# Kernel optimization log

Hardware: AMD Instinct MI355X
Metric: run time of the kernel (lower is better)

The kernel has to match this reference:

```python
import jax, jax.numpy as jnp
import numpy as np

N_EMBD = 768
N_HEAD = 12
HEAD_DIM = N_EMBD // N_HEAD


def setup_inputs() -> dict:
    key = jax.random.key(0)
    k1, k2, k3, k4, k5 = jax.random.split(key, 5)
    B, T, C = 8, 1024, N_EMBD
    s = 0.02
    return {
        "x": jax.random.normal(k1, (B, T, C), dtype=jnp.float32),
        "w_attn": jax.random.normal(k2, (C, 3 * C), dtype=jnp.float32) * s,
        "b_attn": jnp.zeros((3 * C,), dtype=jnp.float32),
        "w_proj": jax.random.normal(k3, (C, C), dtype=jnp.float32) * s,
        "b_proj": jnp.zeros((C,), dtype=jnp.float32),
    }


def reference(x, w_attn, b_attn, w_proj, b_proj):
    B, T, C = x.shape
    H, D = N_HEAD, HEAD_DIM
    qkv = x @ w_attn + b_attn                      # [B,T,3C]
    q, k, v = jnp.split(qkv, 3, axis=-1)
    # [B,H,T,D]
    q = q.reshape(B, T, H, D).transpose(0, 2, 1, 3)
    k = k.reshape(B, T, H, D).transpose(0, 2, 1, 3)
    v = v.reshape(B, T, H, D).transpose(0, 2, 1, 3)
    att = jnp.einsum("bhqd,bhkd->bhqk", q, k) / jnp.sqrt(jnp.float32(D))
    causal = jnp.tril(jnp.ones((T, T), dtype=bool))
    att = jnp.where(causal[None, None], att, jnp.float32(-jnp.inf))
    att = jax.nn.softmax(att, axis=-1)
    y = jnp.einsum("bhqk,bhkd->bhqd", att, v)      # [B,H,T,D]
    y = y.transpose(0, 2, 1, 3).reshape(B, T, C)
    return y @ w_proj + b_proj
```

## Files before the change

### kernel.cpp

```cpp
#include <hip/hip_runtime.h>
#include <hip/hip_bf16.h>
#include <math.h>
#include <type_traits>

#define BATCH 8
#define SEQ   1024
#define NEMBD 768
#define NHEAD 12
#define HDIM  64
#define TC    (3 * NEMBD)

typedef __attribute__((ext_vector_type(4))) float f32x4;
typedef __attribute__((ext_vector_type(8))) short s16x8;

__device__ __forceinline__ unsigned short f2bf(float f) {
    return __builtin_bit_cast(unsigned short, __float2bfloat16(f));
}

__device__ __forceinline__ void gload_lds16(const void* g, void* l) {
    __builtin_amdgcn_global_load_lds(
        (const __attribute__((address_space(1))) void*)g,
        (__attribute__((address_space(3))) void*)l, 16, 0, 0);
}

__global__ __launch_bounds__(256) void prep_kernel(
    const float* __restrict__ x,
    const float* __restrict__ w_attn,
    const float* __restrict__ w_proj,
    unsigned short* __restrict__ xb,
    unsigned short* __restrict__ waT,
    unsigned short* __restrict__ wpT)
{
    const int bid = blockIdx.x, tid = threadIdx.x;
    if (bid < 3072) {
        const int i = (bid * 256 + tid) * 8;
        float4 a = *(const float4*)(x + i);
        float4 b = *(const float4*)(x + i + 4);
        s16x8 v;
        v[0] = f2bf(a.x); v[1] = f2bf(a.y); v[2] = f2bf(a.z); v[3] = f2bf(a.w);
        v[4] = f2bf(b.x); v[5] = f2bf(b.y); v[6] = f2bf(b.z); v[7] = f2bf(b.w);
        *(s16x8*)(xb + i) = v;
        return;
    }
    __shared__ float t[32][33];
    const float* w; unsigned short* wT; int K, N, bx, by;
    if (bid < 4800) {
        const int r = bid - 3072;
        bx = r % 72; by = r / 72; w = w_attn; wT = waT; K = NEMBD; N = TC;
    } else {
        const int r = bid - 4800;
        bx = r % 24; by = r / 24; w = w_proj; wT = wpT; K = NEMBD; N = NEMBD;
    }
    const int tx = tid & 31, ty = tid >> 5;
    const int n0 = bx * 32, k0 = by * 32;
    #pragma unroll
    for (int i = 0; i < 4; ++i)
        t[ty + i * 8][tx] = w[(size_t)(k0 + ty + i * 8) * N + n0 + tx];
    __syncthreads();
    #pragma unroll
    for (int i = 0; i < 4; ++i)
        wT[(size_t)(n0 + ty + i * 8) * K + k0 + tx] = f2bf(t[tx][ty + i * 8]);
}

__global__ __launch_bounds__(512) void gemm_proj256_kernel(
    const unsigned short* __restrict__ A,
    const unsigned short* __restrict__ Bt,
    const float* __restrict__ bias,
    float* __restrict__ C,
    int M, int N, int K, int nbn)
{
    constexpr int BUF = 24576;
    __shared__ __align__(16) char SM[3 * BUF];

    const int tid  = threadIdx.x;
    const int w    = tid >> 6, lane = tid & 63;
    const int lr   = lane & 15, lg = lane >> 4;
    const int wr   = w >> 1, wc = w & 1;

    const int swz = (blockIdx.x & 7) * (gridDim.x >> 3) + (blockIdx.x >> 3);
    const int bm = (swz / nbn) * 256, bn = (swz % nbn) * 128;

    const int srow = tid >> 2;
    const int gcol = ((tid & 3) ^ ((srow >> 1) & 3)) * 8;
    const unsigned short* Ag = A  + (size_t)(bm + srow) * K + gcol;
    const unsigned short* Bg = Bt + (size_t)(bn + srow) * K + gcol;

    const int NT = K >> 5;

    f32x4 acc[4][4];
    #pragma unroll
    for (int m = 0; m < 4; ++m)
        #pragma unroll
        for (int n = 0; n < 4; ++n) acc[m][n] = (f32x4){0.f, 0.f, 0.f, 0.f};

    auto stage = [&](int t) {
        const int k0 = t << 5;
        char* buf = SM + (t % 3) * BUF;
        gload_lds16(Ag + k0,                   buf + tid * 16);
        gload_lds16(Ag + (size_t)128 * K + k0, buf + 8192 + tid * 16);
        gload_lds16(Bg + k0,                   buf + 16384 + tid * 16);
    };

    stage(0);
    stage(1);
    asm volatile("s_waitcnt vmcnt(3)" ::: "memory");
    __builtin_amdgcn_sched_barrier(0);
    __builtin_amdgcn_s_barrier();
    __builtin_amdgcn_sched_barrier(0);

    for (int t = 0; t < NT; ++t) {
        const char* buf = SM + (t % 3) * BUF;
        const bool more = (t + 2 < NT);
        if (more) stage(t + 2);

        s16x8 af[4], bfr[4];
        #pragma unroll
        for (int m = 0; m < 4; ++m) {
            const int ar = wr * 64 + m * 16 + lr;
            af[m] = *(const s16x8*)(buf + ar * 64 + ((lg ^ ((ar >> 1) & 3)) * 16));
        }
        #pragma unroll
        for (int n = 0; n < 4; ++n) {
            const int br = wc * 64 + n * 16 + lr;
            bfr[n] = *(const s16x8*)(buf + 16384 + br * 64
                                         + ((lg ^ ((br >> 1) & 3)) * 16));
        }

        __builtin_amdgcn_s_setprio(1);
        #pragma unroll
        for (int m = 0; m < 4; ++m)
            #pragma unroll
            for (int n = 0; n < 4; ++n)
                acc[m][n] = __builtin_amdgcn_mfma_f32_16x16x32_bf16(
                    af[m], bfr[n], acc[m][n], 0, 0, 0);
        __builtin_amdgcn_s_setprio(0);

        if (more) asm volatile("s_waitcnt vmcnt(3)" ::: "memory");
        else      asm volatile("s_waitcnt vmcnt(0)" ::: "memory");
        __builtin_amdgcn_sched_barrier(0);
        __builtin_amdgcn_s_barrier();
        __builtin_amdgcn_sched_barrier(0);
    }

    #pragma unroll
    for (int n = 0; n < 4; ++n) {
        const int col = bn + wc * 64 + n * 16 + lr;
        const float bv = bias[col];
        #pragma unroll
        for (int m = 0; m < 4; ++m) {
            const int row0 = bm + wr * 64 + m * 16 + lg * 4;
            #pragma unroll
            for (int r = 0; r < 4; ++r)
                C[(size_t)(row0 + r) * N + col] = acc[m][n][r] + bv;
        }
    }
}

__global__ __launch_bounds__(512) void gemm_qkv256_kernel(
    const unsigned short* __restrict__ A,
    const unsigned short* __restrict__ Bt,
    const float* __restrict__ bias,
    unsigned short* __restrict__ Qb,
    unsigned short* __restrict__ Kb,
    unsigned short* __restrict__ Vtb,
    int M, int K, int nbn)
{
    constexpr int BUF = 24576;
    __shared__ __align__(16) char SM[3 * BUF];

    const int tid  = threadIdx.x;
    const int w    = tid >> 6, lane = tid & 63;
    const int lr   = lane & 15, lg = lane >> 4;
    const int wr   = w >> 1, wc = w & 1;

    const int swz = (blockIdx.x & 7) * (gridDim.x >> 3) + (blockIdx.x >> 3);
    const int bm = (swz / nbn) * 256, bn = (swz % nbn) * 128;

    const int srow = tid >> 2;
    const int gcol = ((tid & 3) ^ ((srow >> 1) & 3)) * 8;
    const unsigned short* Ag = A  + (size_t)(bm + srow) * K + gcol;
    const unsigned short* Bg = Bt + (size_t)(bn + srow) * K + gcol;

    const int NT = K >> 5;

    f32x4 acc[4][4];
    #pragma unroll
    for (int m = 0; m < 4; ++m)
        #pragma unroll
        for (int n = 0; n < 4; ++n) acc[m][n] = (f32x4){0.f, 0.f, 0.f, 0.f};

    auto stage = [&](int t) {
        const int k0 = t << 5;
        char* buf = SM + (t % 3) * BUF;
        gload_lds16(Ag + k0,                   buf + tid * 16);
        gload_lds16(Ag + (size_t)128 * K + k0, buf + 8192 + tid * 16);
        gload_lds16(Bg + k0,                   buf + 16384 + tid * 16);
    };

    stage(0);
    stage(1);
    asm volatile("s_waitcnt vmcnt(3)" ::: "memory");
    __builtin_amdgcn_sched_barrier(0);
    __builtin_amdgcn_s_barrier();
    __builtin_amdgcn_sched_barrier(0);

    for (int t = 0; t < NT; ++t) {
        const char* buf = SM + (t % 3) * BUF;
        const bool more = (t + 2 < NT);
        if (more) stage(t + 2);

        s16x8 af[4], bfr[4];
        #pragma unroll
        for (int m = 0; m < 4; ++m) {
            const int ar = wr * 64 + m * 16 + lr;
            af[m] = *(const s16x8*)(buf + ar * 64 + ((lg ^ ((ar >> 1) & 3)) * 16));
        }
        #pragma unroll
        for (int n = 0; n < 4; ++n) {
            const int br = wc * 64 + n * 16 + lr;
            bfr[n] = *(const s16x8*)(buf + 16384 + br * 64
                                         + ((lg ^ ((br >> 1) & 3)) * 16));
        }

        __builtin_amdgcn_s_setprio(1);
        #pragma unroll
        for (int m = 0; m < 4; ++m)
            #pragma unroll
            for (int n = 0; n < 4; ++n)
                acc[m][n] = __builtin_amdgcn_mfma_f32_16x16x32_bf16(
                    af[m], bfr[n], acc[m][n], 0, 0, 0);
        __builtin_amdgcn_s_setprio(0);

        if (more) asm volatile("s_waitcnt vmcnt(3)" ::: "memory");
        else      asm volatile("s_waitcnt vmcnt(0)" ::: "memory");
        __builtin_amdgcn_sched_barrier(0);
        __builtin_amdgcn_s_barrier();
        __builtin_amdgcn_sched_barrier(0);
    }

    char* Ep = SM + w * 8192;

    const int region = bn / NEMBD;
    const int hh = ((bn % NEMBD) >> 6) + wc;
    const int row0 = bm + wr * 64;
    const int bb = row0 >> 10, t0 = row0 & 1023;
    const float scl = (region == 0) ? 0.1803368801111354f : 1.0f;

    float bvn[4];
    #pragma unroll
    for (int n = 0; n < 4; ++n) bvn[n] = bias[bn + wc * 64 + n * 16 + lr];

    if (region == 2) {
        #pragma unroll
        for (int m = 0; m < 4; ++m)
            #pragma unroll
            for (int n = 0; n < 4; ++n) {
                ushort4 pk;
                pk.x = f2bf(acc[m][n][0] + bvn[n]);
                pk.y = f2bf(acc[m][n][1] + bvn[n]);
                pk.z = f2bf(acc[m][n][2] + bvn[n]);
                pk.w = f2bf(acc[m][n][3] + bvn[n]);
                const int row = n * 16 + lr;
                const int lc  = m * 2 + (lg >> 1);
                *(ushort4*)(Ep + row * 128 + ((lc ^ (lr & 7)) * 16)
                               + (lg & 1) * 8) = pk;
            }
    } else {
        #pragma unroll
        for (int m = 0; m < 4; ++m)
            #pragma unroll
            for (int n = 0; n < 4; ++n)
                #pragma unroll
                for (int r = 0; r < 4; ++r) {
                    const int row = m * 16 + lg * 4 + r;
                    const int lc  = n * 2 + (lr >> 3);
                    *(unsigned short*)(Ep + row * 128
                        + ((lc ^ (row & 7)) * 16) + (lr & 7) * 2) =
                        f2bf((acc[m][n][r] + bvn[n]) * scl);
                }
    }
    asm volatile("s_waitcnt lgkmcnt(0)" ::: "memory");
    __builtin_amdgcn_sched_barrier(0);

    const int rr0 = lane >> 3;
    const int cc  = lane & 7;
    if (region == 2) {
        unsigned short* dst = Vtb + (((size_t)bb * NHEAD + hh) * HDIM) * SEQ + t0;
        #pragma unroll
        for (int it = 0; it < 8; ++it) {
            const int d = it * 8 + rr0;
            s16x8 v = *(const s16x8*)(Ep + d * 128 + ((cc ^ (d & 7)) * 16));
            *(s16x8*)(dst + (size_t)d * SEQ + cc * 8) = v;
        }
    } else {
        unsigned short* dst = (region == 0 ? Qb : Kb)
                            + ((size_t)bb * NHEAD + hh) * SEQ * HDIM;
        #pragma unroll
        for (int it = 0; it < 8; ++it) {
            const int t = it * 8 + rr0;
            s16x8 v = *(const s16x8*)(Ep + t * 128 + ((cc ^ (t & 7)) * 16));
            *(s16x8*)(dst + (size_t)(t0 + t) * HDIM + cc * 8) = v;
        }
    }
}

__global__ __launch_bounds__(256) void attn_mfma_kernel(
    const unsigned short* __restrict__ Qb,
    const unsigned short* __restrict__ Kb,
    const unsigned short* __restrict__ Vtb,
    unsigned short* __restrict__ y)
{
    const int bid  = blockIdx.x;
    const int xcd  = bid & 7;
    const int grp  = bid >> 3;
    const int pair = grp & 7;
    const int bh   = xcd + 8 * (grp >> 3);
    const int b    = bh / NHEAD, h = bh % NHEAD;

    const int tid  = threadIdx.x;
    const int w    = tid >> 6;
    const int lane = tid & 63;
    const int lr   = lane & 15;
    const int lg   = lane >> 4;

    __shared__ __align__(16) unsigned short Ks[2][64 * 72];
    __shared__ __align__(16) unsigned short Vs[2][64 * 72];
    __shared__ __align__(16) unsigned short Ps[4][16][72];

    const unsigned short* Kg = Kb  + (size_t)bh * SEQ * HDIM;
    const unsigned short* Vg = Vtb + (size_t)bh * HDIM * SEQ;

    const int sr = tid >> 2;
    const int sc = (tid & 3) * 16;
    const unsigned short* Kgr = Kg + (size_t)sr * HDIM + sc;
    const unsigned short* Vgr = Vg + (size_t)sr * SEQ  + sc;
    const int woff = sr * 72 + sc;

    auto process = [&](int qt) {
        const unsigned short* Qg =
            Qb + ((size_t)bh * SEQ + qt * 64 + w * 16) * HDIM;
        s16x8 qf[2];
        #pragma unroll
        for (int kc = 0; kc < 2; ++kc)
            qf[kc] = *(const s16x8*)(Qg + (size_t)lr * HDIM + kc * 32 + lg * 8);

        f32x4 acc[4];
        #pragma unroll
        for (int df = 0; df < 4; ++df) acc[df] = (f32x4){0.f, 0.f, 0.f, 0.f};
        float lrow = 0.f;

        const int NT   = qt + 1;
        const int qrow = qt * 64 + w * 16 + lr;

        s16x8 krA = *(const s16x8*)(Kgr);
        s16x8 krB = *(const s16x8*)(Kgr + 8);
        s16x8 vrA = *(const s16x8*)(Vgr);
        s16x8 vrB = *(const s16x8*)(Vgr + 8);

        for (int kt = 0; kt < NT; ++kt) {
            const int cb = kt & 1;
            *(s16x8*)(&Ks[cb][woff])     = krA;
            *(s16x8*)(&Ks[cb][woff] + 8) = krB;
            *(s16x8*)(&Vs[cb][woff])     = vrA;
            *(s16x8*)(&Vs[cb][woff] + 8) = vrB;
            if (kt + 1 < NT) {
                krA = *(const s16x8*)(Kgr + (size_t)(kt + 1) * 64 * HDIM);
                krB = *(const s16x8*)(Kgr + (size_t)(kt + 1) * 64 * HDIM + 8);
                vrA = *(const s16x8*)(Vgr + (kt + 1) * 64);
                vrB = *(const s16x8*)(Vgr + (kt + 1) * 64 + 8);
            }
            asm volatile("s_waitcnt lgkmcnt(0)" ::: "memory");
            __builtin_amdgcn_sched_barrier(0);
            __builtin_amdgcn_s_barrier();
            __builtin_amdgcn_sched_barrier(0);

            f32x4 sf[4];
            __builtin_amdgcn_s_setprio(1);
            #pragma unroll
            for (int s = 0; s < 4; ++s) {
                const unsigned short* kr = &Ks[cb][(s * 16 + lr) * 72 + lg * 8];
                s16x8 a0 = *(const s16x8*)(kr);
                s16x8 a1 = *(const s16x8*)(kr + 32);
                sf[s] = __builtin_amdgcn_mfma_f32_16x16x32_bf16(
                    a0, qf[0], (f32x4){0.f, 0.f, 0.f, 0.f}, 0, 0, 0);
                sf[s] = __builtin_amdgcn_mfma_f32_16x16x32_bf16(a1, qf[1], sf[s], 0, 0, 0);
            }
            __builtin_amdgcn_s_setprio(0);

            float sv[4][4];
            #pragma unroll
            for (int s = 0; s < 4; ++s)
                #pragma unroll
                for (int r = 0; r < 4; ++r)
                    sv[s][r] = sf[s][r];
            if (kt == NT - 1) {
                const int kbase = kt * 64;
                #pragma unroll
                for (int s = 0; s < 4; ++s)
                    #pragma unroll
                    for (int r = 0; r < 4; ++r)
                        if (kbase + s * 16 + lg * 4 + r > qrow)
                            sv[s][r] = -INFINITY;
            }

            #pragma unroll
            for (int s = 0; s < 4; ++s) {
                float p0 = exp2f(sv[s][0]);
                float p1 = exp2f(sv[s][1]);
                float p2 = exp2f(sv[s][2]);
                float p3 = exp2f(sv[s][3]);
                lrow += (p0 + p1) + (p2 + p3);
                ushort4 pk;
                pk.x = f2bf(p0); pk.y = f2bf(p1); pk.z = f2bf(p2); pk.w = f2bf(p3);
                *(ushort4*)&Ps[w][lr][s * 16 + lg * 4] = pk;
            }

            asm volatile("s_waitcnt lgkmcnt(0)" ::: "memory");
            __builtin_amdgcn_sched_barrier(0);
            s16x8 pa[2];
            #pragma unroll
            for (int kc = 0; kc < 2; ++kc)
                pa[kc] = *(const s16x8*)&Ps[w][lr][kc * 32 + lg * 8];

            __builtin_amdgcn_s_setprio(1);
            #pragma unroll
            for (int df = 0; df < 4; ++df) {
                const unsigned short* vr = &Vs[cb][(df * 16 + lr) * 72 + lg * 8];
                s16x8 va0 = *(const s16x8*)(vr);
                s16x8 va1 = *(const s16x8*)(vr + 32);
                acc[df] = __builtin_amdgcn_mfma_f32_16x16x32_bf16(va0, pa[0], acc[df], 0, 0, 0);
                acc[df] = __builtin_amdgcn_mfma_f32_16x16x32_bf16(va1, pa[1], acc[df], 0, 0, 0);
            }
            __builtin_amdgcn_s_setprio(0);
        }

        lrow += __shfl_xor(lrow, 16, 64);
        lrow += __shfl_xor(lrow, 32, 64);
        const float inv = 1.f / lrow;
        const int t = qt * 64 + w * 16 + lr;
        unsigned short* yp = y + ((size_t)(b * SEQ) + t) * NEMBD + h * HDIM;
        #pragma unroll
        for (int df = 0; df < 4; ++df) {
            ushort4 pk;
            pk.x = f2bf(acc[df][0] * inv);
            pk.y = f2bf(acc[df][1] * inv);
            pk.z = f2bf(acc[df][2] * inv);
            pk.w = f2bf(acc[df][3] * inv);
            *(ushort4*)(yp + df * 16 + lg * 4) = pk;
        }
        __builtin_amdgcn_s_barrier();
        __builtin_amdgcn_sched_barrier(0);
    };

    process(15 - pair);
    process(pair);
}

extern "C" void kernel_launch(void* const* d_in, const int* in_sizes, int n_in,
                              void* d_out, int out_size, void* d_ws, size_t ws_size,
                              hipStream_t stream)
{
    const float* x      = (const float*)d_in[0];
    const float* w_attn = (const float*)d_in[1];
    const float* b_attn = (const float*)d_in[2];
    const float* w_proj = (const float*)d_in[3];
    const float* b_proj = (const float*)d_in[4];
    float* out = (float*)d_out;

    const int M = BATCH * SEQ;
    const size_t NQKV = (size_t)M * NEMBD;

    unsigned short* xb  = (unsigned short*)d_ws;
    unsigned short* waT = xb  + NQKV;
    unsigned short* wpT = waT + (size_t)TC * NEMBD;
    unsigned short* Qb  = wpT + (size_t)NEMBD * NEMBD;
    unsigned short* Kb  = Qb  + NQKV;
    unsigned short* Vtb = Kb  + NQKV;
    unsigned short* yb  = Vtb + NQKV;

    prep_kernel<<<5376, 256, 0, stream>>>(x, w_attn, w_proj, xb, waT, wpT);

    gemm_qkv256_kernel<<<(M / 256) * (TC / 128), 512, 0, stream>>>(
        xb, waT, b_attn, Qb, Kb, Vtb, M, NEMBD, TC / 128);

    attn_mfma_kernel<<<768, 256, 0, stream>>>(Qb, Kb, Vtb, yb);

    gemm_proj256_kernel<<<(M / 256) * (NEMBD / 128), 512, 0, stream>>>(
        yb, wpT, b_proj, out, M, NEMBD, NEMBD, NEMBD / 128);
}
```

Baseline: 102.1 us.

## Halve QKV GEMM block to 256 threads with 128x64 per-wave tiles

The QKV GEMM now uses 4 waves of 256 threads, each computing a 128x64 output tile (8x4 MFMA accumulators) instead of 8 waves with 64x64 tiles. Loads are restructured so each thread issues 6 LDS-direct loads per stage, and the wait counts change to match. The epilogue writes the two 64-row halves one after another through the per-wave LDS scratch. The goal is more MFMA work per LDS fragment read and less barrier overhead, at the cost of doubled accumulator registers and a launch bound that targets 2 blocks per CU.

```diff
diff --git a/kernel.cpp b/kernel.cpp
--- a/kernel.cpp
+++ b/kernel.cpp
@@ -156,7 +156,7 @@
     }
 }
 
-__global__ __launch_bounds__(512) void gemm_qkv256_kernel(
+__global__ __launch_bounds__(256, 2) void gemm_qkv256_kernel(
     const unsigned short* __restrict__ A,
     const unsigned short* __restrict__ Bt,
     const float* __restrict__ bias,
@@ -183,23 +183,27 @@
 
     const int NT = K >> 5;
 
-    f32x4 acc[4][4];
-    #pragma unroll
-    for (int m = 0; m < 4; ++m)
+    f32x4 acc[8][4];
+    #pragma unroll
+    for (int m = 0; m < 8; ++m)
         #pragma unroll
         for (int n = 0; n < 4; ++n) acc[m][n] = (f32x4){0.f, 0.f, 0.f, 0.f};
 
     auto stage = [&](int t) {
         const int k0 = t << 5;
         char* buf = SM + (t % 3) * BUF;
-        gload_lds16(Ag + k0,                   buf + tid * 16);
-        gload_lds16(Ag + (size_t)128 * K + k0, buf + 8192 + tid * 16);
-        gload_lds16(Bg + k0,                   buf + 16384 + tid * 16);
+        #pragma unroll
+        for (int p = 0; p < 4; ++p)
+            gload_lds16(Ag + (size_t)(p * 64) * K + k0, buf + p * 4096 + tid * 16);
+        #pragma unroll
+        for (int p = 0; p < 2; ++p)
+            gload_lds16(Bg + (size_t)(p * 64) * K + k0,
+                        buf + 16384 + p * 4096 + tid * 16);
     };
 
     stage(0);
     stage(1);
-    asm volatile("s_waitcnt vmcnt(3)" ::: "memory");
+    asm volatile("s_waitcnt vmcnt(6)" ::: "memory");
     __builtin_amdgcn_sched_barrier(0);
     __builtin_amdgcn_s_barrier();
     __builtin_amdgcn_sched_barrier(0);
@@ -209,10 +213,10 @@
         const bool more = (t + 2 < NT);
         if (more) stage(t + 2);
 
-        s16x8 af[4], bfr[4];
-        #pragma unroll
-        for (int m = 0; m < 4; ++m) {
-            const int ar = wr * 64 + m * 16 + lr;
+        s16x8 af[8], bfr[4];
+        #pragma unroll
+        for (int m = 0; m < 8; ++m) {
+            const int ar = wr * 128 + m * 16 + lr;
             af[m] = *(const s16x8*)(buf + ar * 64 + ((lg ^ ((ar >> 1) & 3)) * 16));
         }
         #pragma unroll
@@ -224,14 +228,14 @@
 
         __builtin_amdgcn_s_setprio(1);
         #pragma unroll
-        for (int m = 0; m < 4; ++m)
+        for (int m = 0; m < 8; ++m)
             #pragma unroll
             for (int n = 0; n < 4; ++n)
                 acc[m][n] = __builtin_amdgcn_mfma_f32_16x16x32_bf16(
                     af[m], bfr[n], acc[m][n], 0, 0, 0);
         __builtin_amdgcn_s_setprio(0);
 
-        if (more) asm volatile("s_waitcnt vmcnt(3)" ::: "memory");
+        if (more) asm volatile("s_waitcnt vmcnt(6)" ::: "memory");
         else      asm volatile("s_waitcnt vmcnt(0)" ::: "memory");
         __builtin_amdgcn_sched_barrier(0);
         __builtin_amdgcn_s_barrier();
@@ -242,64 +246,73 @@
 
     const int region = bn / NEMBD;
     const int hh = ((bn % NEMBD) >> 6) + wc;
-    const int row0 = bm + wr * 64;
-    const int bb = row0 >> 10, t0 = row0 & 1023;
     const float scl = (region == 0) ? 0.1803368801111354f : 1.0f;
 
     float bvn[4];
     #pragma unroll
     for (int n = 0; n < 4; ++n) bvn[n] = bias[bn + wc * 64 + n * 16 + lr];
 
-    if (region == 2) {
-        #pragma unroll
-        for (int m = 0; m < 4; ++m)
-            #pragma unroll
-            for (int n = 0; n < 4; ++n) {
-                ushort4 pk;
-                pk.x = f2bf(acc[m][n][0] + bvn[n]);
-                pk.y = f2bf(acc[m][n][1] + bvn[n]);
-                pk.z = f2bf(acc[m][n][2] + bvn[n]);
-                pk.w = f2bf(acc[m][n][3] + bvn[n]);
-                const int row = n * 16 + lr;
-                const int lc  = m * 2 + (lg >> 1);
-                *(ushort4*)(Ep + row * 128 + ((lc ^ (lr & 7)) * 16)
-                               + (lg & 1) * 8) = pk;
-            }
-    } else {
-        #pragma unroll
-        for (int m = 0; m < 4; ++m)
-            #pragma unroll
-            for (int n = 0; n < 4; ++n)
+    #pragma unroll
+    for (int c = 0; c < 2; ++c) {
+        if (c) {
+            asm volatile("s_waitcnt lgkmcnt(0)" ::: "memory");
+            __builtin_amdgcn_sched_barrier(0);
+        }
+        const int row0 = bm + wr * 128 + c * 64;
+        const int bb = row0 >> 10, t0 = row0 & 1023;
+
+        if (region == 2) {
+            #pragma unroll
+            for (int m4 = 0; m4 < 4; ++m4)
                 #pragma unroll
-                for (int r = 0; r < 4; ++r) {
-                    const int row = m * 16 + lg * 4 + r;
-                    const int lc  = n * 2 + (lr >> 3);
-                    *(unsigned short*)(Ep + row * 128
-                        + ((lc ^ (row & 7)) * 16) + (lr & 7) * 2) =
-                        f2bf((acc[m][n][r] + bvn[n]) * scl);
+                for (int n = 0; n < 4; ++n) {
+                    const f32x4 a = acc[c * 4 + m4][n];
+                    ushort4 pk;
+                    pk.x = f2bf(a[0] + bvn[n]);
+                    pk.y = f2bf(a[1] + bvn[n]);
+                    pk.z = f2bf(a[2] + bvn[n]);
+                    pk.w = f2bf(a[3] + bvn[n]);
+                    const int row = n * 16 + lr;
+                    const int lc  = m4 * 2 + (lg >> 1);
+                    *(ushort4*)(Ep + row * 128 + ((lc ^ (lr & 7)) * 16)
+                                   + (lg & 1) * 8) = pk;
                 }
-    }
-    asm volatile("s_waitcnt lgkmcnt(0)" ::: "memory");
-    __builtin_amdgcn_sched_barrier(0);
-
-    const int rr0 = lane >> 3;
-    const int cc  = lane & 7;
-    if (region == 2) {
-        unsigned short* dst = Vtb + (((size_t)bb * NHEAD + hh) * HDIM) * SEQ + t0;
-        #pragma unroll
-        for (int it = 0; it < 8; ++it) {
-            const int d = it * 8 + rr0;
-            s16x8 v = *(const s16x8*)(Ep + d * 128 + ((cc ^ (d & 7)) * 16));
-            *(s16x8*)(dst + (size_t)d * SEQ + cc * 8) = v;
-        }
-    } else {
-        unsigned short* dst = (region == 0 ? Qb : Kb)
-                            + ((size_t)bb * NHEAD + hh) * SEQ * HDIM;
-        #pragma unroll
-        for (int it = 0; it < 8; ++it) {
-            const int t = it * 8 + rr0;
-            s16x8 v = *(const s16x8*)(Ep + t * 128 + ((cc ^ (t & 7)) * 16));
-            *(s16x8*)(dst + (size_t)(t0 + t) * HDIM + cc * 8) = v;
+        } else {
+            #pragma unroll
+            for (int m4 = 0; m4 < 4; ++m4)
+                #pragma unroll
+                for (int n = 0; n < 4; ++n)
+                    #pragma unroll
+                    for (int r = 0; r < 4; ++r) {
+                        const int row = m4 * 16 + lg * 4 + r;
+                        const int lc  = n * 2 + (lr >> 3);
+                        *(unsigned short*)(Ep + row * 128
+                            + ((lc ^ (row & 7)) * 16) + (lr & 7) * 2) =
+                            f2bf((acc[c * 4 + m4][n][r] + bvn[n]) * scl);
+                    }
+        }
+        asm volatile("s_waitcnt lgkmcnt(0)" ::: "memory");
+        __builtin_amdgcn_sched_barrier(0);
+
+        const int rr0 = lane >> 3;
+        const int cc  = lane & 7;
+        if (region == 2) {
+            unsigned short* dst = Vtb + (((size_t)bb * NHEAD + hh) * HDIM) * SEQ + t0;
+            #pragma unroll
+            for (int it = 0; it < 8; ++it) {
+                const int d = it * 8 + rr0;
+                s16x8 v = *(const s16x8*)(Ep + d * 128 + ((cc ^ (d & 7)) * 16));
+                *(s16x8*)(dst + (size_t)d * SEQ + cc * 8) = v;
+            }
+        } else {
+            unsigned short* dst = (region == 0 ? Qb : Kb)
+                                + ((size_t)bb * NHEAD + hh) * SEQ * HDIM;
+            #pragma unroll
+            for (int it = 0; it < 8; ++it) {
+                const int t = it * 8 + rr0;
+                s16x8 v = *(const s16x8*)(Ep + t * 128 + ((cc ^ (t & 7)) * 16));
+                *(s16x8*)(dst + (size_t)(t0 + t) * HDIM + cc * 8) = v;
+            }
         }
     }
 }
@@ -480,7 +493,7 @@
 
     prep_kernel<<<5376, 256, 0, stream>>>(x, w_attn, w_proj, xb, waT, wpT);
 
-    gemm_qkv256_kernel<<<(M / 256) * (TC / 128), 512, 0, stream>>>(
+    gemm_qkv256_kernel<<<(M / 256) * (TC / 128), 256, 0, stream>>>(
         xb, waT, b_attn, Qb, Kb, Vtb, M, NEMBD, TC / 128);
 
     attn_mfma_kernel<<<768, 256, 0, stream>>>(Qb, Kb, Vtb, yb);
```

Result: slower. 104.8 us (+2.7%).

## Share K/V tiles between paired query tiles in a single causal pass

Applied to the files above, without the earlier changes.

Rather than running two sequential passes over keys for the query tiles 15-pair and pair, the kernel now loads each K/V tile into shared memory once and applies it to both query tiles. The second tile's work is skipped once past its causal limit. This roughly halves K/V global loads and staging barriers per block and removes the barrier between the two passes. The cost is doubled accumulator and Q fragment registers, which may lower occupancy, and a per-iteration branch for the shorter tile.

```diff
diff --git a/kernel.cpp b/kernel.cpp
--- a/kernel.cpp
+++ b/kernel.cpp
@@ -336,124 +336,144 @@
     const unsigned short* Vgr = Vg + (size_t)sr * SEQ  + sc;
     const int woff = sr * 72 + sc;
 
-    auto process = [&](int qt) {
-        const unsigned short* Qg =
-            Qb + ((size_t)bh * SEQ + qt * 64 + w * 16) * HDIM;
-        s16x8 qf[2];
-        #pragma unroll
-        for (int kc = 0; kc < 2; ++kc)
-            qf[kc] = *(const s16x8*)(Qg + (size_t)lr * HDIM + kc * 32 + lg * 8);
-
-        f32x4 acc[4];
-        #pragma unroll
-        for (int df = 0; df < 4; ++df) acc[df] = (f32x4){0.f, 0.f, 0.f, 0.f};
-        float lrow = 0.f;
-
-        const int NT   = qt + 1;
-        const int qrow = qt * 64 + w * 16 + lr;
-
-        s16x8 krA = *(const s16x8*)(Kgr);
-        s16x8 krB = *(const s16x8*)(Kgr + 8);
-        s16x8 vrA = *(const s16x8*)(Vgr);
-        s16x8 vrB = *(const s16x8*)(Vgr + 8);
-
-        for (int kt = 0; kt < NT; ++kt) {
-            const int cb = kt & 1;
-            *(s16x8*)(&Ks[cb][woff])     = krA;
-            *(s16x8*)(&Ks[cb][woff] + 8) = krB;
-            *(s16x8*)(&Vs[cb][woff])     = vrA;
-            *(s16x8*)(&Vs[cb][woff] + 8) = vrB;
-            if (kt + 1 < NT) {
-                krA = *(const s16x8*)(Kgr + (size_t)(kt + 1) * 64 * HDIM);
-                krB = *(const s16x8*)(Kgr + (size_t)(kt + 1) * 64 * HDIM + 8);
-                vrA = *(const s16x8*)(Vgr + (kt + 1) * 64);
-                vrB = *(const s16x8*)(Vgr + (kt + 1) * 64 + 8);
-            }
-            asm volatile("s_waitcnt lgkmcnt(0)" ::: "memory");
-            __builtin_amdgcn_sched_barrier(0);
-            __builtin_amdgcn_s_barrier();
-            __builtin_amdgcn_sched_barrier(0);
-
-            f32x4 sf[4];
-            __builtin_amdgcn_s_setprio(1);
-            #pragma unroll
-            for (int s = 0; s < 4; ++s) {
-                const unsigned short* kr = &Ks[cb][(s * 16 + lr) * 72 + lg * 8];
-                s16x8 a0 = *(const s16x8*)(kr);
-                s16x8 a1 = *(const s16x8*)(kr + 32);
-                sf[s] = __builtin_amdgcn_mfma_f32_16x16x32_bf16(
-                    a0, qf[0], (f32x4){0.f, 0.f, 0.f, 0.f}, 0, 0, 0);
-                sf[s] = __builtin_amdgcn_mfma_f32_16x16x32_bf16(a1, qf[1], sf[s], 0, 0, 0);
-            }
-            __builtin_amdgcn_s_setprio(0);
-
-            float sv[4][4];
+    const int qtA = 15 - pair, qtB = pair;
+    const int NT  = qtA + 1;
+    const int qrowA = qtA * 64 + w * 16 + lr;
+    const int qrowB = qtB * 64 + w * 16 + lr;
+
+    const unsigned short* QgA = Qb + ((size_t)bh * SEQ + qtA * 64 + w * 16) * HDIM;
+    const unsigned short* QgB = Qb + ((size_t)bh * SEQ + qtB * 64 + w * 16) * HDIM;
+    s16x8 qfA[2], qfB[2];
+    #pragma unroll
+    for (int kc = 0; kc < 2; ++kc) {
+        qfA[kc] = *(const s16x8*)(QgA + (size_t)lr * HDIM + kc * 32 + lg * 8);
+        qfB[kc] = *(const s16x8*)(QgB + (size_t)lr * HDIM + kc * 32 + lg * 8);
+    }
+
+    f32x4 accA[4], accB[4];
+    #pragma unroll
+    for (int df = 0; df < 4; ++df) {
+        accA[df] = (f32x4){0.f, 0.f, 0.f, 0.f};
+        accB[df] = (f32x4){0.f, 0.f, 0.f, 0.f};
+    }
+    float lrowA = 0.f, lrowB = 0.f;
+
+    auto tile_work = [&](const s16x8* qf, f32x4* acc, float& lrow,
+                         int qrow, bool domask, int kbase, int cb) {
+        f32x4 sf[4];
+        __builtin_amdgcn_s_setprio(1);
+        #pragma unroll
+        for (int s = 0; s < 4; ++s) {
+            const unsigned short* kr = &Ks[cb][(s * 16 + lr) * 72 + lg * 8];
+            s16x8 a0 = *(const s16x8*)(kr);
+            s16x8 a1 = *(const s16x8*)(kr + 32);
+            sf[s] = __builtin_amdgcn_mfma_f32_16x16x32_bf16(
+                a0, qf[0], (f32x4){0.f, 0.f, 0.f, 0.f}, 0, 0, 0);
+            sf[s] = __builtin_amdgcn_mfma_f32_16x16x32_bf16(a1, qf[1], sf[s], 0, 0, 0);
+        }
+        __builtin_amdgcn_s_setprio(0);
+
+        if (domask) {
             #pragma unroll
             for (int s = 0; s < 4; ++s)
                 #pragma unroll
                 for (int r = 0; r < 4; ++r)
-                    sv[s][r] = sf[s][r];
-            if (kt == NT - 1) {
-                const int kbase = kt * 64;
-                #pragma unroll
-                for (int s = 0; s < 4; ++s)
-                    #pragma unroll
-                    for (int r = 0; r < 4; ++r)
-                        if (kbase + s * 16 + lg * 4 + r > qrow)
-                            sv[s][r] = -INFINITY;
-            }
-
-            #pragma unroll
-            for (int s = 0; s < 4; ++s) {
-                float p0 = exp2f(sv[s][0]);
-                float p1 = exp2f(sv[s][1]);
-                float p2 = exp2f(sv[s][2]);
-                float p3 = exp2f(sv[s][3]);
-                lrow += (p0 + p1) + (p2 + p3);
-                ushort4 pk;
-                pk.x = f2bf(p0); pk.y = f2bf(p1); pk.z = f2bf(p2); pk.w = f2bf(p3);
-                *(ushort4*)&Ps[w][lr][s * 16 + lg * 4] = pk;
-            }
-
-            asm volatile("s_waitcnt lgkmcnt(0)" ::: "memory");
-            __builtin_amdgcn_sched_barrier(0);
-            s16x8 pa[2];
-            #pragma unroll
-            for (int kc = 0; kc < 2; ++kc)
-                pa[kc] = *(const s16x8*)&Ps[w][lr][kc * 32 + lg * 8];
-
-            __builtin_amdgcn_s_setprio(1);
-            #pragma unroll
-            for (int df = 0; df < 4; ++df) {
-                const unsigned short* vr = &Vs[cb][(df * 16 + lr) * 72 + lg * 8];
-                s16x8 va0 = *(const s16x8*)(vr);
-                s16x8 va1 = *(const s16x8*)(vr + 32);
-                acc[df] = __builtin_amdgcn_mfma_f32_16x16x32_bf16(va0, pa[0], acc[df], 0, 0, 0);
-                acc[df] = __builtin_amdgcn_mfma_f32_16x16x32_bf16(va1, pa[1], acc[df], 0, 0, 0);
-            }
-            __builtin_amdgcn_s_setprio(0);
-        }
-
-        lrow += __shfl_xor(lrow, 16, 64);
-        lrow += __shfl_xor(lrow, 32, 64);
-        const float inv = 1.f / lrow;
-        const int t = qt * 64 + w * 16 + lr;
+                    if (kbase + s * 16 + lg * 4 + r > qrow)
+                        sf[s][r] = -INFINITY;
+        }
+
+        #pragma unroll
+        for (int s = 0; s < 4; ++s) {
+            float p0 = exp2f(sf[s][0]);
+            float p1 = exp2f(sf[s][1]);
+            float p2 = exp2f(sf[s][2]);
+            float p3 = exp2f(sf[s][3]);
+            lrow += (p0 + p1) + (p2 + p3);
+            ushort4 pk;
+            pk.x = f2bf(p0); pk.y = f2bf(p1); pk.z = f2bf(p2); pk.w = f2bf(p3);
+            *(ushort4*)&Ps[w][lr][s * 16 + lg * 4] = pk;
+        }
+
+        asm volatile("s_waitcnt lgkmcnt(0)" ::: "memory");
+        __builtin_amdgcn_sched_barrier(0);
+        s16x8 pa[2];
+        #pragma unroll
+        for (int kc = 0; kc < 2; ++kc)
+            pa[kc] = *(const s16x8*)&Ps[w][lr][kc * 32 + lg * 8];
+
+        __builtin_amdgcn_s_setprio(1);
+        #pragma unroll
+        for (int df = 0; df < 4; ++df) {
+            const unsigned short* vr = &Vs[cb][(df * 16 + lr) * 72 + lg * 8];
+            s16x8 va0 = *(const s16x8*)(vr);
+            s16x8 va1 = *(const s16x8*)(vr + 32);
+            acc[df] = __builtin_amdgcn_mfma_f32_16x16x32_bf16(va0, pa[0], acc[df], 0, 0, 0);
+            acc[df] = __builtin_amdgcn_mfma_f32_16x16x32_bf16(va1, pa[1], acc[df], 0, 0, 0);
+        }
+        __builtin_amdgcn_s_setprio(0);
+    };
+
+    s16x8 krA = *(const s16x8*)(Kgr);
+    s16x8 krB = *(const s16x8*)(Kgr + 8);
+    s16x8 vrA = *(const s16x8*)(Vgr);
+    s16x8 vrB = *(const s16x8*)(Vgr + 8);
+
+    for (int kt = 0; kt < NT; ++kt) {
+        const int cb = kt & 1;
+        *(s16x8*)(&Ks[cb][woff])     = krA;
+        *(s16x8*)(&Ks[cb][woff] + 8) = krB;
+        *(s16x8*)(&Vs[cb][woff])     = vrA;
+        *(s16x8*)(&Vs[cb][woff] + 8) = vrB;
+        if (kt + 1 < NT) {
+            krA = *(const s16x8*)(Kgr + (size_t)(kt + 1) * 64 * HDIM);
+            krB = *(const s16x8*)(Kgr + (size_t)(kt + 1) * 64 * HDIM + 8);
+            vrA = *(const s16x8*)(Vgr + (kt + 1) * 64);
+            vrB = *(const s16x8*)(Vgr + (kt + 1) * 64 + 8);
+        }
+        asm volatile("s_waitcnt lgkmcnt(0)" ::: "memory");
+        __builtin_amdgcn_sched_barrier(0);
+        __builtin_amdgcn_s_barrier();
+        __builtin_amdgcn_sched_barrier(0);
+
+        tile_work(qfA, accA, lrowA, qrowA, kt == NT - 1, kt * 64, cb);
+        if (kt <= qtB)
+            tile_work(qfB, accB, lrowB, qrowB, kt == qtB, kt * 64, cb);
+    }
+
+    {
+        float l = lrowA;
+        l += __shfl_xor(l, 16, 64);
+        l += __shfl_xor(l, 32, 64);
+        const float inv = 1.f / l;
+        const int t = qtA * 64 + w * 16 + lr;
         unsigned short* yp = y + ((size_t)(b * SEQ) + t) * NEMBD + h * HDIM;
         #pragma unroll
         for (int df = 0; df < 4; ++df) {
             ushort4 pk;
-            pk.x = f2bf(acc[df][0] * inv);
-            pk.y = f2bf(acc[df][1] * inv);
-            pk.z = f2bf(acc[df][2] * inv);
-            pk.w = f2bf(acc[df][3] * inv);
+            pk.x = f2bf(accA[df][0] * inv);
+            pk.y = f2bf(accA[df][1] * inv);
+            pk.z = f2bf(accA[df][2] * inv);
+            pk.w = f2bf(accA[df][3] * inv);
             *(ushort4*)(yp + df * 16 + lg * 4) = pk;
         }
-        __builtin_amdgcn_s_barrier();
-        __builtin_amdgcn_sched_barrier(0);
-    };
-
-    process(15 - pair);
-    process(pair);
+    }
+    {
+        float l = lrowB;
+        l += __shfl_xor(l, 16, 64);
+        l += __shfl_xor(l, 32, 64);
+        const float inv = 1.f / l;
+        const int t = qtB * 64 + w * 16 + lr;
+        unsigned short* yp = y + ((size_t)(b * SEQ) + t) * NEMBD + h * HDIM;
+        #pragma unroll
+        for (int df = 0; df < 4; ++df) {
+            ushort4 pk;
+            pk.x = f2bf(accB[df][0] * inv);
+            pk.y = f2bf(accB[df][1] * inv);
+            pk.z = f2bf(accB[df][2] * inv);
+            pk.w = f2bf(accB[df][3] * inv);
+            *(ushort4*)(yp + df * 16 + lg * 4) = pk;
+        }
+    }
 }
 
 extern "C" void kernel_launch(void* const* d_in, const int* in_sizes, int n_in,
```

Result: no change. 102.9 us (+0.8%).
